# Performance work log

Measured on AMD Instinct MI355X. Metric: run time of the kernel, lower is better.

Reference implementation:

```python
import jax, jax.numpy as jnp
import numpy as np
from jax import lax

N_OBS = 16_777_216
N_STATES = 12  # 1 + n_states per module __init__
TOTAL_EXP_READ_DEPTH = 25.0


def setup_inputs() -> dict:
    key = jax.random.key(0)
    k_obs, k_states, k_means, k_phis = jax.random.split(key, 4)
    # NB-distributed counts as floats (log_prob is evaluated at float counts in torch too)
    obs = jax.random.randint(k_obs, (N_OBS,), 0, 50).astype(jnp.float32)
    states = jax.random.randint(k_states, (N_OBS,), 0, N_STATES, dtype=jnp.int64)
    # Parameters as in init_emission: means ~ U(0, depth), phis ~ U(0,1)
    state_means = TOTAL_EXP_READ_DEPTH * jax.random.uniform(k_means, (N_STATES,), dtype=jnp.float32)
    state_phis = jax.random.uniform(k_phis, (N_STATES,), dtype=jnp.float32)
    return {"obs": obs, "states": states, "state_means": state_means, "state_phis": state_phis}


def _nb_log_prob(obs, means, phis):
    # torch NegativeBinomial(total_count=r, probs=p) with r=means, p=means/(means+phis):
    # log_prob(k) = r*log(1-p) + k*log(p) + lgamma(k+r) - lgamma(k+1) - lgamma(r)
    log_denom = jnp.log(means + phis)
    log_p = jnp.log(means) - log_denom        # log probs
    log_1mp = jnp.log(phis) - log_denom       # log(1 - probs)
    return (means * log_1mp + obs * log_p
            + lax.lgamma(obs + means) - lax.lgamma(obs + 1.0) - lax.lgamma(means))


def reference(obs, states, state_means, state_phis):
    # one_hot @ params in the original is just a gather
    means = state_means[states]
    phis = state_phis[states]
    return jnp.sum(_nb_log_prob(obs, means, phis))
```

## Files before the change

kernel.cpp:

```cpp
#include <hip/hip_runtime.h>

#define N_STATES 12
#define MAX_OBS 50
#define TABLE_SIZE (N_STATES * MAX_OBS)
#define SUM_BLOCKS 512
#define SUM_THREADS 512


__global__ void build_table_kernel(const float* __restrict__ state_means,
                                   const float* __restrict__ state_phis,
                                   float* __restrict__ table) {
    int t = blockIdx.x * blockDim.x + threadIdx.x;
    if (t >= TABLE_SIZE) return;
    int s = t / MAX_OBS;
    int o = t % MAX_OBS;
    double m  = (double)state_means[s];
    double ph = (double)state_phis[s];
    double ob = (double)o;
    double log_denom = log(m + ph);
    double log_p   = log(m)  - log_denom;
    double log_1mp = log(ph) - log_denom;
    double lp = m * log_1mp + ob * log_p
              + lgamma(ob + m) - lgamma(ob + 1.0) - lgamma(m);
    table[t] = (float)lp;
}

__global__ void __launch_bounds__(SUM_THREADS, 4) nb_hist_kernel(const float* __restrict__ obs,
                                                                 const int* __restrict__ states,
                                                                 const float* __restrict__ table,
                                                                 float* __restrict__ partials,
                                                                 int n) {
    __shared__ unsigned int hist[TABLE_SIZE];
    for (int i = threadIdx.x; i < TABLE_SIZE; i += blockDim.x)
        hist[i] = 0u;
    __syncthreads();

    const int tid = blockIdx.x * blockDim.x + threadIdx.x;
    const int nthreads = gridDim.x * blockDim.x;
    const int n4 = n >> 2;
    const float4* __restrict__ obs4 = (const float4*)obs;
    const int4*  __restrict__ st4  = (const int4*)states;

    #pragma unroll 4
    for (int i = tid; i < n4; i += nthreads) {
        float4 o = obs4[i];
        int4   s = st4[i];
        atomicAdd(&hist[s.x * MAX_OBS + (int)o.x], 1u);
        atomicAdd(&hist[s.y * MAX_OBS + (int)o.y], 1u);
        atomicAdd(&hist[s.z * MAX_OBS + (int)o.z], 1u);
        atomicAdd(&hist[s.w * MAX_OBS + (int)o.w], 1u);
    }
    for (int i = (n4 << 2) + tid; i < n; i += nthreads)
        atomicAdd(&hist[states[i] * MAX_OBS + (int)obs[i]], 1u);
    __syncthreads();

    float acc = 0.0f;
    for (int i = threadIdx.x; i < TABLE_SIZE; i += blockDim.x)
        acc += (float)hist[i] * table[i];

    #pragma unroll
    for (int off = 32; off > 0; off >>= 1)
        acc += __shfl_down(acc, off, 64);

    __shared__ float wsum[SUM_THREADS / 64];
    const int lane = threadIdx.x & 63;
    const int wid  = threadIdx.x >> 6;
    if (lane == 0) wsum[wid] = acc;
    __syncthreads();
    if (threadIdx.x == 0) {
        float s = 0.0f;
        #pragma unroll
        for (int w = 0; w < SUM_THREADS / 64; ++w) s += wsum[w];
        partials[blockIdx.x] = s;
    }
}

__global__ void __launch_bounds__(SUM_BLOCKS) final_reduce_kernel(const float* __restrict__ partials,
                                                                  float* __restrict__ out) {
    float acc = partials[threadIdx.x];
    #pragma unroll
    for (int off = 32; off > 0; off >>= 1)
        acc += __shfl_down(acc, off, 64);
    __shared__ float wsum[SUM_BLOCKS / 64];
    const int lane = threadIdx.x & 63;
    const int wid  = threadIdx.x >> 6;
    if (lane == 0) wsum[wid] = acc;
    __syncthreads();
    if (threadIdx.x == 0) {
        float s = 0.0f;
        #pragma unroll
        for (int w = 0; w < SUM_BLOCKS / 64; ++w) s += wsum[w];
        *out = s;
    }
}

extern "C" void kernel_launch(void* const* d_in, const int* in_sizes, int n_in,
                              void* d_out, int out_size, void* d_ws, size_t ws_size,
                              hipStream_t stream) {
    const float* obs         = (const float*)d_in[0];
    const int*   states      = (const int*)d_in[1];
    const float* state_means = (const float*)d_in[2];
    const float* state_phis  = (const float*)d_in[3];
    float* out      = (float*)d_out;
    float* table    = (float*)d_ws;
    float* partials = table + TABLE_SIZE;
    const int n = in_sizes[0];

    build_table_kernel<<<dim3((TABLE_SIZE + 255) / 256), dim3(256), 0, stream>>>(
        state_means, state_phis, table);

    nb_hist_kernel<<<dim3(SUM_BLOCKS), dim3(SUM_THREADS), 0, stream>>>(
        obs, states, table, partials, n);

    final_reduce_kernel<<<dim3(1), dim3(SUM_BLOCKS), 0, stream>>>(partials, out);
}
```

Before: 31.73 us.

## Replicate shared histogram into sub-histograms and retune grid to smaller blocks

Each block now keeps four copies of the shared-memory histogram, and groups of 16 threads write to different copies, which is meant to cut LDS atomic contention. The copies are summed before the dot product with the log-prob table. The launch moves to 2048 blocks of 256 threads, and the final reduction loops over the larger partials array. The cost is more shared memory per block and more partials to reduce.

```diff
diff --git a/kernel.cpp b/kernel.cpp
--- a/kernel.cpp
+++ b/kernel.cpp
@@ -3,8 +3,9 @@
 #define N_STATES 12
 #define MAX_OBS 50
 #define TABLE_SIZE (N_STATES * MAX_OBS)
-#define SUM_BLOCKS 512
-#define SUM_THREADS 512
+#define NSUB 4
+#define SUM_BLOCKS 2048
+#define SUM_THREADS 256
 
 
 __global__ void build_table_kernel(const float* __restrict__ state_means,
@@ -25,13 +26,13 @@
     table[t] = (float)lp;
 }
 
-__global__ void __launch_bounds__(SUM_THREADS, 4) nb_hist_kernel(const float* __restrict__ obs,
+__global__ void __launch_bounds__(SUM_THREADS, 8) nb_hist_kernel(const float* __restrict__ obs,
                                                                  const int* __restrict__ states,
                                                                  const float* __restrict__ table,
                                                                  float* __restrict__ partials,
                                                                  int n) {
-    __shared__ unsigned int hist[TABLE_SIZE];
-    for (int i = threadIdx.x; i < TABLE_SIZE; i += blockDim.x)
+    __shared__ unsigned int hist[NSUB * TABLE_SIZE];
+    for (int i = threadIdx.x; i < NSUB * TABLE_SIZE; i += blockDim.x)
         hist[i] = 0u;
     __syncthreads();
 
@@ -41,22 +42,28 @@
     const float4* __restrict__ obs4 = (const float4*)obs;
     const int4*  __restrict__ st4  = (const int4*)states;
 
+    unsigned int* mh = hist + ((threadIdx.x >> 4) & (NSUB - 1)) * TABLE_SIZE;
+
     #pragma unroll 4
     for (int i = tid; i < n4; i += nthreads) {
         float4 o = obs4[i];
         int4   s = st4[i];
-        atomicAdd(&hist[s.x * MAX_OBS + (int)o.x], 1u);
-        atomicAdd(&hist[s.y * MAX_OBS + (int)o.y], 1u);
-        atomicAdd(&hist[s.z * MAX_OBS + (int)o.z], 1u);
-        atomicAdd(&hist[s.w * MAX_OBS + (int)o.w], 1u);
+        atomicAdd(&mh[s.x * MAX_OBS + (int)o.x], 1u);
+        atomicAdd(&mh[s.y * MAX_OBS + (int)o.y], 1u);
+        atomicAdd(&mh[s.z * MAX_OBS + (int)o.z], 1u);
+        atomicAdd(&mh[s.w * MAX_OBS + (int)o.w], 1u);
     }
     for (int i = (n4 << 2) + tid; i < n; i += nthreads)
-        atomicAdd(&hist[states[i] * MAX_OBS + (int)obs[i]], 1u);
+        atomicAdd(&mh[states[i] * MAX_OBS + (int)obs[i]], 1u);
     __syncthreads();
 
     float acc = 0.0f;
-    for (int i = threadIdx.x; i < TABLE_SIZE; i += blockDim.x)
-        acc += (float)hist[i] * table[i];
+    for (int i = threadIdx.x; i < TABLE_SIZE; i += blockDim.x) {
+        unsigned int c = hist[i];
+        #pragma unroll
+        for (int k = 1; k < NSUB; ++k) c += hist[k * TABLE_SIZE + i];
+        acc += (float)c * table[i];
+    }
 
     #pragma unroll
     for (int off = 32; off > 0; off >>= 1)
@@ -75,23 +82,21 @@
     }
 }
 
-__global__ void __launch_bounds__(SUM_BLOCKS) final_reduce_kernel(const float* __restrict__ partials,
-                                                                  float* __restrict__ out) {
-    float acc = partials[threadIdx.x];
+__global__ void __launch_bounds__(256) final_reduce_kernel(const float* __restrict__ partials,
+                                                           float* __restrict__ out) {
+    float acc = 0.0f;
+    for (int i = threadIdx.x; i < SUM_BLOCKS; i += 256)
+        acc += partials[i];
     #pragma unroll
     for (int off = 32; off > 0; off >>= 1)
         acc += __shfl_down(acc, off, 64);
-    __shared__ float wsum[SUM_BLOCKS / 64];
+    __shared__ float wsum[4];
     const int lane = threadIdx.x & 63;
     const int wid  = threadIdx.x >> 6;
     if (lane == 0) wsum[wid] = acc;
     __syncthreads();
-    if (threadIdx.x == 0) {
-        float s = 0.0f;
-        #pragma unroll
-        for (int w = 0; w < SUM_BLOCKS / 64; ++w) s += wsum[w];
-        *out = s;
-    }
+    if (threadIdx.x == 0)
+        *out = wsum[0] + wsum[1] + wsum[2] + wsum[3];
 }
 
 extern "C" void kernel_launch(void* const* d_in, const int* in_sizes, int n_in,
@@ -112,5 +117,5 @@
     nb_hist_kernel<<<dim3(SUM_BLOCKS), dim3(SUM_THREADS), 0, stream>>>(
         obs, states, table, partials, n);
 
-    final_reduce_kernel<<<dim3(1), dim3(SUM_BLOCKS), 0, stream>>>(partials, out);
+    final_reduce_kernel<<<dim3(1), dim3(256), 0, stream>>>(partials, out);
 }
```

New measurement: 35.01 us. +10.3%, slower.
